# Kernel tuning notes

Hardware: AMD Instinct MI355X
Metric: run time of the kernel (lower is better)

The kernel has to match this reference:

```python
import jax, jax.numpy as jnp
import numpy as np

SAMPLE_NUM = 8
TIMESPAN = 4
EPS = 1e-8  # torch cosine_similarity eps


def setup_inputs() -> dict:
    key = jax.random.key(0)
    ks = jax.random.split(key, 6)
    S, N, H, Z = 512, 1024, 128, 64
    return {
        "all_h": jax.random.normal(ks[0], (S, N, H), jnp.float32),
        "all_z": jax.random.normal(ks[1], (S, N, Z), jnp.float32),
        "Wh": jax.random.normal(ks[2], (H, H), jnp.float32) / np.sqrt(H),
        "bh": jnp.zeros((H,), jnp.float32),
        "Wz": jax.random.normal(ks[3], (H, Z), jnp.float32) / np.sqrt(Z),
        "bz": jnp.zeros((H,), jnp.float32),
        "Wphi": jax.random.normal(ks[4], (H, H), jnp.float32) / np.sqrt(H),
        "bphi": jnp.zeros((H,), jnp.float32),
    }


def reference(all_h, all_z, Wh, bh, Wz, bz, Wphi, bphi):
    # graph pooling: mean over nodes, then linear projection to h_dim
    h_pool = jnp.mean(all_h, axis=1) @ Wh.T + bh  # [S, H]
    z_pool = jnp.mean(all_z, axis=1) @ Wz.T + bz  # [S, H]
    S = z_pool.shape[0]

    neg_dist = S // 6
    end = S - SAMPLE_NUM - neg_dist - TIMESPAN + 2
    start = S // 8 if S // 8 < end else 0
    cnt = end - start

    # distance term: mean over t of squared distance to global mean
    gmean = jnp.mean(z_pool, axis=0)
    distance = jnp.sum((z_pool - gmean) ** 2) / S

    # gather positive + negative samples for every (t_sample, step)
    t = jnp.arange(start, end)               # [T]
    i = jnp.arange(1, TIMESPAN + 1)          # [I]
    n = jnp.arange(SAMPLE_NUM)               # [M]
    offs = jnp.where(n == 0, 0, neg_dist + n - 1)            # [M]
    idx = t[:, None, None] + i[None, :, None] + offs[None, None, :]  # [T, I, M]
    enc = z_pool[idx]                        # [T, I, M, H]

    # context projection (single fixed phi, applied per step)
    c_phi = h_pool[start:end] @ Wphi.T + bphi  # [T, H]

    # cosine similarity, log-softmax over the M samples, positive at index 0
    num = jnp.einsum('timf,tf->tim', enc, c_phi)
    denom = (jnp.maximum(jnp.linalg.norm(enc, axis=-1), EPS)
             * jnp.maximum(jnp.linalg.norm(c_phi, axis=-1)[:, None, None], EPS))
    sim = num / denom                        # [T, I, M]
    nce = jnp.sum(jax.nn.log_softmax(sim, axis=-1)[..., 0])
    nce_loss = nce / (-1.0 * cnt * TIMESPAN)
    return (nce_loss, distance)
```

## Files before the change

### kernel.cpp

```cpp
#include <hip/hip_runtime.h>
#include <math.h>

#define S_DIM 512
#define N_NODE 1024
#define H_DIM 128
#define Z_DIM 64
#define T_START 64
#define T_CNT 353
#define NEG_DIST 85
#define TIMESPAN 4
#define M_SAMP 8
#define EPS_F 1e-8f
#define DIST_B 4

typedef float f4 __attribute__((ext_vector_type(4)));

__global__ __launch_bounds__(256) void pool_proj_kernel(
        const float* __restrict__ all_h, const float* __restrict__ all_z,
        const float* __restrict__ Wh,   const float* __restrict__ bh,
        const float* __restrict__ Wz,   const float* __restrict__ bz,
        const float* __restrict__ Wphi, const float* __restrict__ bphi,
        float* __restrict__ c_phi, float* __restrict__ cnorm,
        float* __restrict__ z_pool, float* __restrict__ znorm) {
    __shared__ __align__(16) f4 red4[256];
    __shared__ __align__(16) float mrow[H_DIM];
    __shared__ __align__(16) float hrow[H_DIM];
    __shared__ float sred[H_DIM];
    const int tid = threadIdx.x;
    const int b = blockIdx.x;
    const int o = tid >> 1, half = tid & 1;

    if (b < T_CNT) {
        const int s = T_START + b;
        const int h4 = tid & 31, grp = tid >> 5;
        const f4* p = (const f4*)(all_h + (size_t)s * N_NODE * H_DIM);
        f4 acc = {0.f, 0.f, 0.f, 0.f};
        #pragma unroll 8
        for (int n = grp; n < N_NODE; n += 8)
            acc += __builtin_nontemporal_load(&p[n * 32 + h4]);
        red4[grp * 32 + h4] = acc;
        __syncthreads();
        for (int st = 4; st >= 1; st >>= 1) {
            if (grp < st) red4[grp * 32 + h4] += red4[(grp + st) * 32 + h4];
            __syncthreads();
        }
        if (grp == 0)
            *(f4*)&mrow[h4 * 4] = red4[h4] * (1.0f / (float)N_NODE);
        __syncthreads();

        {
            const float* w = Wh + o * H_DIM + half * 64;
            const float* x = mrow + half * 64;
            float ps = 0.f;
            #pragma unroll 8
            for (int k = 0; k < 64; ++k) ps = fmaf(x[k], w[k], ps);
            ps += __shfl_xor(ps, 1);
            if (half == 0) hrow[o] = ps + bh[o];
        }
        __syncthreads();
        {
            const float* w = Wphi + o * H_DIM + half * 64;
            const float* x = hrow + half * 64;
            float ps = 0.f;
            #pragma unroll 8
            for (int k = 0; k < 64; ++k) ps = fmaf(x[k], w[k], ps);
            ps += __shfl_xor(ps, 1);
            if (half == 0) {
                float cv = ps + bphi[o];
                c_phi[b * H_DIM + o] = cv;
                sred[o] = cv * cv;
            }
        }
        __syncthreads();
        for (int st = 64; st >= 1; st >>= 1) {
            if (tid < st) sred[tid] += sred[tid + st];
            __syncthreads();
        }
        if (tid == 0) cnorm[b] = fmaxf(sqrtf(sred[0]), EPS_F);
    } else {
        const int s = b - T_CNT;
        const int h4 = tid & 15, grp = tid >> 4;
        const f4* p = (const f4*)(all_z + (size_t)s * N_NODE * Z_DIM);
        f4 acc = {0.f, 0.f, 0.f, 0.f};
        #pragma unroll 8
        for (int n = grp; n < N_NODE; n += 16)
            acc += __builtin_nontemporal_load(&p[n * 16 + h4]);
        red4[grp * 16 + h4] = acc;
        __syncthreads();
        for (int st = 8; st >= 1; st >>= 1) {
            if (grp < st) red4[grp * 16 + h4] += red4[(grp + st) * 16 + h4];
            __syncthreads();
        }
        if (grp == 0)
            *(f4*)&mrow[h4 * 4] = red4[h4] * (1.0f / (float)N_NODE);
        __syncthreads();

        const float* w = Wz + o * Z_DIM + half * 32;
        const float* x = mrow + half * 32;
        float ps = 0.f;
        #pragma unroll 8
        for (int k = 0; k < 32; ++k) ps = fmaf(x[k], w[k], ps);
        ps += __shfl_xor(ps, 1);
        if (half == 0) {
            float zp = ps + bz[o];
            z_pool[s * H_DIM + o] = zp;
            sred[o] = zp * zp;
        }
        __syncthreads();
        for (int st = 64; st >= 1; st >>= 1) {
            if (tid < st) sred[tid] += sred[tid + st];
            __syncthreads();
        }
        if (tid == 0) znorm[s] = sqrtf(sred[0]);
    }
}

__global__ __launch_bounds__(128) void nce_dist_kernel(
        const float* __restrict__ c_phi, const float* __restrict__ cnorm,
        const float* __restrict__ z_pool, const float* __restrict__ znorm,
        float* __restrict__ partial, float* __restrict__ dsum,
        float* __restrict__ dsq) {
    const int b = blockIdx.x, tid = threadIdx.x;
    if (b < T_CNT) {
        __shared__ float c[H_DIM];
        __shared__ float sims[32];
        __shared__ float contrib[4];
        c[tid] = c_phi[b * H_DIM + tid];
        __syncthreads();
        const float cn = cnorm[b];
        const int pr = tid >> 2, l4 = tid & 3;
        const int i = pr >> 3, m = pr & 7;
        const int off = (m == 0) ? 0 : (NEG_DIST + m - 1);
        const int row = T_START + b + (i + 1) + off;
        const float* zr = z_pool + row * H_DIM;
        float num = 0.f;
        #pragma unroll 8
        for (int k = l4 * 32; k < l4 * 32 + 32; ++k) num = fmaf(zr[k], c[k], num);
        num += __shfl_xor(num, 1);
        num += __shfl_xor(num, 2);
        if (l4 == 0) sims[pr] = num / (fmaxf(znorm[row], EPS_F) * cn);
        __syncthreads();
        if (tid < 4) {
            const float* sm = sims + tid * 8;
            float mx = sm[0];
            #pragma unroll
            for (int k = 1; k < M_SAMP; ++k) mx = fmaxf(mx, sm[k]);
            float se = 0.f;
            #pragma unroll
            for (int k = 0; k < M_SAMP; ++k) se += expf(sm[k] - mx);
            contrib[tid] = sm[0] - mx - logf(se);
        }
        __syncthreads();
        if (tid == 0)
            partial[b] = contrib[0] + contrib[1] + contrib[2] + contrib[3];
    } else {
        const int ch = b - T_CNT;
        const int s0 = ch * (S_DIM / DIST_B);
        float sum = 0.f, sq = 0.f;
        for (int s = s0; s < s0 + S_DIM / DIST_B; ++s) {
            float v = z_pool[s * H_DIM + tid];
            sum += v;
            sq = fmaf(v, v, sq);
        }
        dsum[ch * H_DIM + tid] = sum;
        dsq[ch * H_DIM + tid] = sq;
    }
}

__global__ __launch_bounds__(512) void final_kernel(
        const float* __restrict__ partial, const float* __restrict__ dsum,
        const float* __restrict__ dsq, float* __restrict__ out) {
    const int tid = threadIdx.x;
    __shared__ float red[512];
    __shared__ float dred[H_DIM];
    red[tid] = (tid < T_CNT) ? partial[tid] : 0.f;
    if (tid < H_DIM) {
        float S = 0.f, Q = 0.f;
        #pragma unroll
        for (int c = 0; c < DIST_B; ++c) {
            S += dsum[c * H_DIM + tid];
            Q += dsq[c * H_DIM + tid];
        }
        dred[tid] = Q - S * S / (float)S_DIM;
    }
    __syncthreads();
    for (int st = 256; st >= 1; st >>= 1) {
        if (tid < st) red[tid] += red[tid + st];
        __syncthreads();
    }
    for (int st = 64; st >= 1; st >>= 1) {
        if (tid < st) dred[tid] += dred[tid + st];
        __syncthreads();
    }
    if (tid == 0) {
        out[0] = red[0] / (-1.0f * (float)T_CNT * (float)TIMESPAN);
        out[1] = dred[0] / (float)S_DIM;
    }
}

extern "C" void kernel_launch(void* const* d_in, const int* in_sizes, int n_in,
                              void* d_out, int out_size, void* d_ws, size_t ws_size,
                              hipStream_t stream) {
    const float* all_h = (const float*)d_in[0];
    const float* all_z = (const float*)d_in[1];
    const float* Wh    = (const float*)d_in[2];
    const float* bh    = (const float*)d_in[3];
    const float* Wz    = (const float*)d_in[4];
    const float* bz    = (const float*)d_in[5];
    const float* Wphi  = (const float*)d_in[6];
    const float* bphi  = (const float*)d_in[7];
    float* out = (float*)d_out;

    float* ws = (float*)d_ws;
    float* c_phi   = ws;
    float* cnorm   = c_phi + T_CNT * H_DIM;
    float* z_pool  = cnorm + T_CNT;
    float* znorm   = z_pool + S_DIM * H_DIM;
    float* partial = znorm + S_DIM;
    float* dsum    = partial + T_CNT;
    float* dsq     = dsum + DIST_B * H_DIM;

    pool_proj_kernel<<<T_CNT + S_DIM, 256, 0, stream>>>(
        all_h, all_z, Wh, bh, Wz, bz, Wphi, bphi, c_phi, cnorm, z_pool, znorm);
    nce_dist_kernel<<<T_CNT + DIST_B, 128, 0, stream>>>(
        c_phi, cnorm, z_pool, znorm, partial, dsum, dsq);
    final_kernel<<<1, 512, 0, stream>>>(partial, dsum, dsq, out);
}
```

Before: 73.79 us.

## Split all_h pooling across node chunks and move projections into NCE kernel

The per-timestep mean over all_h, which reads 512 KB per block, is now split into four node-chunk blocks per timestep, which write partial sums. The Wh/Wphi projections and the c_phi norm move into the NCE kernel, which combines the four partials first. The z pooling blocks come first in the grid. The goal is to shorten the long-tail h blocks and improve load balance and memory-level parallelism. The cost is extra partial-sum traffic and the projection work added to the second kernel. The projection loops are also vectorized with float4.

```diff
diff --git a/kernel.cpp b/kernel.cpp
--- a/kernel.cpp
+++ b/kernel.cpp
@@ -12,73 +12,23 @@
 #define M_SAMP 8
 #define EPS_F 1e-8f
 #define DIST_B 4
+#define H_CHUNKS 4
 
 typedef float f4 __attribute__((ext_vector_type(4)));
 
-__global__ __launch_bounds__(256) void pool_proj_kernel(
+__global__ __launch_bounds__(256) void pool_kernel(
         const float* __restrict__ all_h, const float* __restrict__ all_z,
-        const float* __restrict__ Wh,   const float* __restrict__ bh,
-        const float* __restrict__ Wz,   const float* __restrict__ bz,
-        const float* __restrict__ Wphi, const float* __restrict__ bphi,
-        float* __restrict__ c_phi, float* __restrict__ cnorm,
-        float* __restrict__ z_pool, float* __restrict__ znorm) {
+        const float* __restrict__ Wz, const float* __restrict__ bz,
+        float* __restrict__ z_pool, float* __restrict__ znorm,
+        float* __restrict__ hpart) {
     __shared__ __align__(16) f4 red4[256];
     __shared__ __align__(16) float mrow[H_DIM];
-    __shared__ __align__(16) float hrow[H_DIM];
     __shared__ float sred[H_DIM];
     const int tid = threadIdx.x;
     const int b = blockIdx.x;
-    const int o = tid >> 1, half = tid & 1;
-
-    if (b < T_CNT) {
-        const int s = T_START + b;
-        const int h4 = tid & 31, grp = tid >> 5;
-        const f4* p = (const f4*)(all_h + (size_t)s * N_NODE * H_DIM);
-        f4 acc = {0.f, 0.f, 0.f, 0.f};
-        #pragma unroll 8
-        for (int n = grp; n < N_NODE; n += 8)
-            acc += __builtin_nontemporal_load(&p[n * 32 + h4]);
-        red4[grp * 32 + h4] = acc;
-        __syncthreads();
-        for (int st = 4; st >= 1; st >>= 1) {
-            if (grp < st) red4[grp * 32 + h4] += red4[(grp + st) * 32 + h4];
-            __syncthreads();
-        }
-        if (grp == 0)
-            *(f4*)&mrow[h4 * 4] = red4[h4] * (1.0f / (float)N_NODE);
-        __syncthreads();
-
-        {
-            const float* w = Wh + o * H_DIM + half * 64;
-            const float* x = mrow + half * 64;
-            float ps = 0.f;
-            #pragma unroll 8
-            for (int k = 0; k < 64; ++k) ps = fmaf(x[k], w[k], ps);
-            ps += __shfl_xor(ps, 1);
-            if (half == 0) hrow[o] = ps + bh[o];
-        }
-        __syncthreads();
-        {
-            const float* w = Wphi + o * H_DIM + half * 64;
-            const float* x = hrow + half * 64;
-            float ps = 0.f;
-            #pragma unroll 8
-            for (int k = 0; k < 64; ++k) ps = fmaf(x[k], w[k], ps);
-            ps += __shfl_xor(ps, 1);
-            if (half == 0) {
-                float cv = ps + bphi[o];
-                c_phi[b * H_DIM + o] = cv;
-                sred[o] = cv * cv;
-            }
-        }
-        __syncthreads();
-        for (int st = 64; st >= 1; st >>= 1) {
-            if (tid < st) sred[tid] += sred[tid + st];
-            __syncthreads();
-        }
-        if (tid == 0) cnorm[b] = fmaxf(sqrtf(sred[0]), EPS_F);
-    } else {
-        const int s = b - T_CNT;
+
+    if (b < S_DIM) {
+        const int s = b;
         const int h4 = tid & 15, grp = tid >> 4;
         const f4* p = (const f4*)(all_z + (size_t)s * N_NODE * Z_DIM);
         f4 acc = {0.f, 0.f, 0.f, 0.f};
@@ -95,6 +45,7 @@
             *(f4*)&mrow[h4 * 4] = red4[h4] * (1.0f / (float)N_NODE);
         __syncthreads();
 
+        const int o = tid >> 1, half = tid & 1;
         const float* w = Wz + o * Z_DIM + half * 32;
         const float* x = mrow + half * 32;
         float ps = 0.f;
@@ -112,22 +63,91 @@
             __syncthreads();
         }
         if (tid == 0) znorm[s] = sqrtf(sred[0]);
+    } else {
+        const int b2 = b - S_DIM;
+        const int t = b2 >> 2, ch = b2 & 3;
+        const int s = T_START + t;
+        const int h4 = tid & 31, grp = tid >> 5;
+        const int n0 = ch * (N_NODE / H_CHUNKS);
+        const f4* p = (const f4*)(all_h + (size_t)s * N_NODE * H_DIM);
+        f4 acc = {0.f, 0.f, 0.f, 0.f};
+        #pragma unroll 8
+        for (int n = n0 + grp; n < n0 + N_NODE / H_CHUNKS; n += 8)
+            acc += __builtin_nontemporal_load(&p[n * 32 + h4]);
+        red4[grp * 32 + h4] = acc;
+        __syncthreads();
+        for (int st = 4; st >= 1; st >>= 1) {
+            if (grp < st) red4[grp * 32 + h4] += red4[(grp + st) * 32 + h4];
+            __syncthreads();
+        }
+        if (grp == 0)
+            *(f4*)&hpart[b2 * H_DIM + h4 * 4] = red4[h4];
     }
 }
 
 __global__ __launch_bounds__(128) void nce_dist_kernel(
-        const float* __restrict__ c_phi, const float* __restrict__ cnorm,
+        const float* __restrict__ hpart,
+        const float* __restrict__ Wh,   const float* __restrict__ bh,
+        const float* __restrict__ Wphi, const float* __restrict__ bphi,
         const float* __restrict__ z_pool, const float* __restrict__ znorm,
         float* __restrict__ partial, float* __restrict__ dsum,
         float* __restrict__ dsq) {
     const int b = blockIdx.x, tid = threadIdx.x;
     if (b < T_CNT) {
-        __shared__ float c[H_DIM];
+        __shared__ __align__(16) float mrow[H_DIM];
+        __shared__ __align__(16) float hrow[H_DIM];
+        __shared__ __align__(16) float c[H_DIM];
+        __shared__ float sred[H_DIM];
         __shared__ float sims[32];
         __shared__ float contrib[4];
-        c[tid] = c_phi[b * H_DIM + tid];
-        __syncthreads();
-        const float cn = cnorm[b];
+        __shared__ float s_cn;
+
+        const float* hp = hpart + b * (H_CHUNKS * H_DIM);
+        mrow[tid] = (hp[tid] + hp[H_DIM + tid] + hp[2 * H_DIM + tid] +
+                     hp[3 * H_DIM + tid]) * (1.0f / (float)N_NODE);
+        __syncthreads();
+
+        const int o = tid >> 1, half = tid & 1;
+        {
+            const f4* w4 = (const f4*)(Wh + o * H_DIM + half * 64);
+            const f4* x4 = (const f4*)(mrow + half * 64);
+            float ps = 0.f;
+            #pragma unroll
+            for (int k = 0; k < 16; ++k) {
+                f4 a = w4[k], x = x4[k];
+                ps = fmaf(a.x, x.x, ps); ps = fmaf(a.y, x.y, ps);
+                ps = fmaf(a.z, x.z, ps); ps = fmaf(a.w, x.w, ps);
+            }
+            ps += __shfl_xor(ps, 1);
+            if (half == 0) hrow[o] = ps + bh[o];
+        }
+        __syncthreads();
+        {
+            const f4* w4 = (const f4*)(Wphi + o * H_DIM + half * 64);
+            const f4* x4 = (const f4*)(hrow + half * 64);
+            float ps = 0.f;
+            #pragma unroll
+            for (int k = 0; k < 16; ++k) {
+                f4 a = w4[k], x = x4[k];
+                ps = fmaf(a.x, x.x, ps); ps = fmaf(a.y, x.y, ps);
+                ps = fmaf(a.z, x.z, ps); ps = fmaf(a.w, x.w, ps);
+            }
+            ps += __shfl_xor(ps, 1);
+            if (half == 0) {
+                float cv = ps + bphi[o];
+                c[o] = cv;
+                sred[o] = cv * cv;
+            }
+        }
+        __syncthreads();
+        for (int st = 64; st >= 1; st >>= 1) {
+            if (tid < st) sred[tid] += sred[tid + st];
+            __syncthreads();
+        }
+        if (tid == 0) s_cn = fmaxf(sqrtf(sred[0]), EPS_F);
+        __syncthreads();
+        const float cn = s_cn;
+
         const int pr = tid >> 2, l4 = tid & 3;
         const int i = pr >> 3, m = pr & 7;
         const int off = (m == 0) ? 0 : (NEG_DIST + m - 1);
@@ -212,17 +232,16 @@
     float* out = (float*)d_out;
 
     float* ws = (float*)d_ws;
-    float* c_phi   = ws;
-    float* cnorm   = c_phi + T_CNT * H_DIM;
-    float* z_pool  = cnorm + T_CNT;
+    float* z_pool  = ws;
     float* znorm   = z_pool + S_DIM * H_DIM;
-    float* partial = znorm + S_DIM;
+    float* hpart   = znorm + S_DIM;
+    float* partial = hpart + T_CNT * H_CHUNKS * H_DIM;
     float* dsum    = partial + T_CNT;
     float* dsq     = dsum + DIST_B * H_DIM;
 
-    pool_proj_kernel<<<T_CNT + S_DIM, 256, 0, stream>>>(
-        all_h, all_z, Wh, bh, Wz, bz, Wphi, bphi, c_phi, cnorm, z_pool, znorm);
+    pool_kernel<<<S_DIM + T_CNT * H_CHUNKS, 256, 0, stream>>>(
+        all_h, all_z, Wz, bz, z_pool, znorm, hpart);
     nce_dist_kernel<<<T_CNT + DIST_B, 128, 0, stream>>>(
-        c_phi, cnorm, z_pool, znorm, partial, dsum, dsq);
+        hpart, Wh, bh, Wphi, bphi, z_pool, znorm, partial, dsum, dsq);
     final_kernel<<<1, 512, 0, stream>>>(partial, dsum, dsq, out);
 }
```

Measured after the change: 63.63 us. -13.8%, faster.
